# Optimization experiments

Measured on AMD Instinct MI355X. Metric: run time of the kernel, lower is better.

## Reference

```python
import jax, jax.numpy as jnp
import numpy as np

N, D, H = 100000, 128, 8
C = D // H
E = 800000
NEG_SLOPE = 0.2


def setup_inputs() -> dict:
    key = jax.random.key(0)
    k1, k2, k3, k4, k5, k6 = jax.random.split(key, 6)
    x = jax.random.normal(k1, (N, D), dtype=jnp.float32)
    edge_index = jax.random.randint(k2, (2, E), 0, N, dtype=jnp.int64)
    # GATConv params: shared linear (single node-feature input), per-head attention vectors, bias
    W = jax.random.normal(k3, (D, H * C), dtype=jnp.float32) * (1.0 / np.sqrt(D))
    att_src = jax.random.normal(k4, (H, C), dtype=jnp.float32) * 0.1
    att_dst = jax.random.normal(k5, (H, C), dtype=jnp.float32) * 0.1
    bias = jnp.zeros((H * C,), dtype=jnp.float32)
    return {"x": x, "edge_index": edge_index, "W": W, "att_src": att_src, "att_dst": att_dst, "bias": bias}


def reference(x, edge_index, W, att_src, att_dst, bias):
    # PyG GATConv default: add self-loops
    loops = jnp.tile(jnp.arange(N, dtype=edge_index.dtype), (2, 1))  # [2, N]
    ei = jnp.concatenate([edge_index, loops], axis=1)                # [2, E+N]
    src, dst = ei[0], ei[1]

    h = (x @ W).reshape(N, H, C)                    # [N, H, C]
    a_src = jnp.einsum('nhc,hc->nh', h, att_src)    # [N, H]
    a_dst = jnp.einsum('nhc,hc->nh', h, att_dst)    # [N, H]

    logits = jax.nn.leaky_relu(a_src[src] + a_dst[dst], negative_slope=NEG_SLOPE)  # [Etot, H]

    # segment softmax grouped by destination node (every node has a self-loop -> non-empty)
    mx = jax.ops.segment_max(logits, dst, num_segments=N)   # [N, H]
    ex = jnp.exp(logits - mx[dst])                           # [Etot, H]
    denom = jax.ops.segment_sum(ex, dst, num_segments=N)    # [N, H]
    alpha = ex / (denom[dst] + 1e-16)                        # [Etot, H]

    msg = h[src] * alpha[:, :, None]                         # [Etot, H, C]
    out = jax.ops.segment_sum(msg, dst, num_segments=N)      # [N, H, C]
    out = out.reshape(N, H * C) + bias                       # concat heads
    return out, ei, alpha
```

## Files before the change

kernel.cpp:

```cpp
#include <hip/hip_runtime.h>
#include <hip/hip_bf16.h>
#include <cstdint>

#define N_NODES 100000
#define DIM 128
#define HEADS 8
#define CH 16
#define NEDGE 800000
#define ETOT (NEDGE + N_NODES)
#define NEG_SLOPE 0.2f
#define CAP 64
#define PRE 20

typedef __attribute__((ext_vector_type(8))) short bf16x8;
typedef __attribute__((ext_vector_type(4))) float f32x4;

__device__ __forceinline__ float leaky(float v) {
    return v >= 0.f ? v : NEG_SLOPE * v;
}

__device__ __forceinline__ void split2(float w, ushort& hi, ushort& lo) {
    __hip_bfloat16 bh = __float2bfloat16(w);
    float r = w - __bfloat162float(bh);
    __hip_bfloat16 bl = __float2bfloat16(r);
    hi = *(ushort*)&bh;
    lo = *(ushort*)&bl;
}

#define NCOLS 144
#define LDK   136
#define MT    128
#define EDGE_TPB 512
#define EDGE_BLOCKS ((ETOT + EDGE_TPB - 1) / EDGE_TPB)
#define GEMM_BLOCKS ((N_NODES + MT - 1) / MT)

__global__ __launch_bounds__(512, 4) void fused_kernel(
    const float* __restrict__ x, const float* __restrict__ W,
    const float* __restrict__ att_src, const float* __restrict__ att_dst,
    __hip_bfloat16* __restrict__ h, float* __restrict__ a_src,
    float* __restrict__ a_dst,
    const int* __restrict__ edge_index, float* __restrict__ ei_out,
    int* __restrict__ fill, int* __restrict__ ebuf)
{
    __shared__ ushort Whi[NCOLS * LDK];
    __shared__ ushort Wlo[NCOLS * LDK];
    const int tid = threadIdx.x;

    if (blockIdx.x < EDGE_BLOCKS) {
        const int e = blockIdx.x * EDGE_TPB + tid;
        if (e < ETOT) {
            int s, d;
            if (e < NEDGE) { s = edge_index[e]; d = edge_index[NEDGE + e]; }
            else           { s = d = e - NEDGE; }
            ei_out[e]        = (float)s;
            ei_out[ETOT + e] = (float)d;
            int pos = atomicAdd(&fill[d], 1);
            if (pos < CAP) ebuf[d * CAP + pos] = e;
        }
        return;
    }
    const int bid = blockIdx.x - EDGE_BLOCKS;

    {
        const int n  = tid >> 2;
        const int kq = (tid & 3) * 32;
        #pragma unroll
        for (int j = 0; j < 32; j += 2) {
            const int k = kq + j;
            float w0 = W[(size_t)k * DIM + n];
            float w1 = W[(size_t)(k + 1) * DIM + n];
            ushort h0, l0, h1, l1;
            split2(w0, h0, l0);
            split2(w1, h1, l1);
            *(uint*)&Whi[n * LDK + k] = (uint)h0 | ((uint)h1 << 16);
            *(uint*)&Wlo[n * LDK + k] = (uint)l0 | ((uint)l1 << 16);
        }
    }
    if (tid < 64) {
        const int t  = tid >> 2;
        const int kq = (tid & 3) * 32;
        const int hd = t & 7;
        const float* av = ((t < 8) ? att_src : att_dst) + hd * CH;
        float avr[CH];
        #pragma unroll
        for (int c = 0; c < CH; ++c) avr[c] = av[c];
        const int nrow = 128 + t;
        for (int j = 0; j < 32; j += 2) {
            const int k = kq + j;
            const float* wp0 = &W[(size_t)k * DIM + hd * CH];
            const float* wp1 = wp0 + DIM;
            float s0 = 0.f, s1 = 0.f;
            #pragma unroll
            for (int c = 0; c < CH; ++c) { s0 += wp0[c] * avr[c]; s1 += wp1[c] * avr[c]; }
            ushort h0, l0, h1, l1;
            split2(s0, h0, l0);
            split2(s1, h1, l1);
            *(uint*)&Whi[nrow * LDK + k] = (uint)h0 | ((uint)h1 << 16);
            *(uint*)&Wlo[nrow * LDK + k] = (uint)l0 | ((uint)l1 << 16);
        }
    }
    __syncthreads();

    const int w    = tid >> 6;
    const int lane = tid & 63;
    const int r    = lane & 15;
    const int g    = lane >> 4;
    const long arow = (long)bid * MT + w * 16 + r;
    const bool avalid = arow < N_NODES;

    f32x4 acc[9] = {};
    #pragma unroll
    for (int ks = 0; ks < 4; ++ks) {
        const int k0 = ks * 32 + g * 8;
        float xv[8];
        if (avalid) {
            *(float4*)&xv[0] = *(const float4*)&x[arow * DIM + k0];
            *(float4*)&xv[4] = *(const float4*)&x[arow * DIM + k0 + 4];
        } else {
            #pragma unroll
            for (int j = 0; j < 8; ++j) xv[j] = 0.f;
        }
        bf16x8 ahi, alo;
        #pragma unroll
        for (int j = 0; j < 8; ++j) {
            ushort hb, lb;
            split2(xv[j], hb, lb);
            ahi[j] = (short)hb;
            alo[j] = (short)lb;
        }
        #pragma unroll
        for (int nt = 0; nt < 9; ++nt) {
            const int nr = nt * 16 + r;
            bf16x8 bhi = *(const bf16x8*)&Whi[nr * LDK + k0];
            bf16x8 blo = *(const bf16x8*)&Wlo[nr * LDK + k0];
            acc[nt] = __builtin_amdgcn_mfma_f32_16x16x32_bf16(ahi, bhi, acc[nt], 0, 0, 0);
            acc[nt] = __builtin_amdgcn_mfma_f32_16x16x32_bf16(alo, bhi, acc[nt], 0, 0, 0);
            acc[nt] = __builtin_amdgcn_mfma_f32_16x16x32_bf16(ahi, blo, acc[nt], 0, 0, 0);
        }
    }

    const long orow0 = (long)bid * MT + w * 16 + g * 4;
    #pragma unroll
    for (int q = 0; q < 4; ++q) {
        const long orow = orow0 + q;
        if (orow < N_NODES) {
            #pragma unroll
            for (int nt = 0; nt < 8; ++nt)
                h[orow * DIM + nt * 16 + r] = __float2bfloat16(acc[nt][q]);
            const float av = acc[8][q];
            if (r < 8) a_src[orow * HEADS + r]       = av;
            else       a_dst[orow * HEADS + (r - 8)] = av;
        }
    }
}

__global__ __launch_bounds__(256, 8) void gather_kernel(
    const int* __restrict__ edge_index, const int* __restrict__ fill,
    const int* __restrict__ ebuf, const __hip_bfloat16* __restrict__ h,
    const float* __restrict__ a_src, const float* __restrict__ a_dst,
    const float* __restrict__ bias, float* __restrict__ alpha_out,
    float* __restrict__ out)
{
    const int tid  = threadIdx.x;
    const int lane = tid & 63;
    const int n    = blockIdx.x * 4 + (tid >> 6);
    const int head = lane >> 3, c = lane & 7;
    const int chb  = head * CH + c * 2;

    const int   dn = min(fill[n], CAP);
    const float ad = a_dst[(uint)n * HEADS + head];
    const int   e  = ebuf[(uint)n * CAP + lane];
    int s = 0;
    if (lane < dn) s = (e < NEDGE) ? edge_index[e] : e - NEDGE;

    const char* hb  = (const char*)h;
    const uint  cho = (uint)chb * 2u;
    const int npre = min(dn, PRE);
    unsigned hv[PRE];
    #pragma unroll
    for (int q = 0; q < PRE; ++q) {
        int sq = __shfl(s, q);
        if (q < npre)
            hv[q] = *(const unsigned*)(hb + ((uint)sq * 256u + cho));
    }

    const char* asb = (const char*)a_src;
    const uint  hdo = (uint)(head << 2);
    float lg[8];
    float m = -1e30f;
    #pragma unroll
    for (int k = 0; k < 8; ++k) {
        const int i = c + 8 * k;
        if (i < dn) {
            int si = __shfl(s, i);
            float as = *(const float*)(asb + ((uint)si * 32u + hdo));
            lg[k] = leaky(as + ad);
            m = fmaxf(m, lg[k]);
        }
    }
    #pragma unroll
    for (int off = 1; off < 8; off <<= 1)
        m = fmaxf(m, __shfl_xor(m, off));

    float ex[8];
    float dsum = 0.f;
    #pragma unroll
    for (int k = 0; k < 8; ++k) {
        const int i = c + 8 * k;
        if (i < dn) { ex[k] = __expf(lg[k] - m); dsum += ex[k]; }
    }
    #pragma unroll
    for (int off = 1; off < 8; off <<= 1)
        dsum += __shfl_xor(dsum, off);
    const float rdinv = 1.f / (dsum + 1e-16f);

    float ax = 0.f, ay = 0.f;
    #pragma unroll
    for (int q = 0; q < PRE; ++q) {
        if (q < npre) {
            float exq = __shfl(ex[q >> 3], head * 8 + (q & 7));
            ax += __uint_as_float(hv[q] << 16) * exq;
            ay += __uint_as_float(hv[q] & 0xffff0000u) * exq;
        }
    }
    for (int q = PRE; q < dn; ++q) {
        int sq = __shfl(s, q);
        unsigned hq = *(const unsigned*)(hb + ((uint)sq * 256u + cho));
        float asq = *(const float*)(asb + ((uint)sq * 32u + hdo));
        float exq = __expf(leaky(asq + ad) - m);
        ax += __uint_as_float(hq << 16) * exq;
        ay += __uint_as_float(hq & 0xffff0000u) * exq;
    }
    ax *= rdinv; ay *= rdinv;
    float2 b = *(const float2*)&bias[chb];
    float2 rr; rr.x = ax + b.x; rr.y = ay + b.y;
    *(float2*)&out[(uint)n * DIM + chb] = rr;

    #pragma unroll
    for (int k = 0; k < 8; ++k) {
        const int i = c + 8 * k;
        if (i < dn) {
            int ei = __shfl(e, i);
            alpha_out[(uint)ei * 8u + head] = ex[k] * rdinv;
        }
    }
}

extern "C" void kernel_launch(void* const* d_in, const int* in_sizes, int n_in,
                              void* d_out, int out_size, void* d_ws, size_t ws_size,
                              hipStream_t stream) {
    const float* x          = (const float*)d_in[0];
    const int*   edge_index = (const int*)d_in[1];
    const float* W          = (const float*)d_in[2];
    const float* att_src    = (const float*)d_in[3];
    const float* att_dst    = (const float*)d_in[4];
    const float* bias       = (const float*)d_in[5];

    float* out       = (float*)d_out;
    float* ei_out    = out + (size_t)N_NODES * DIM;
    float* alpha_out = ei_out + 2 * (size_t)ETOT;

    __hip_bfloat16* h = (__hip_bfloat16*)d_ws;
    float* a_src = (float*)(h + (size_t)N_NODES * DIM);
    float* a_dst = a_src + (size_t)N_NODES * HEADS;
    int*   fill  = (int*)(a_dst + (size_t)N_NODES * HEADS);
    int*   ebuf  = fill + N_NODES;

    hipMemsetAsync(fill, 0, (size_t)N_NODES * sizeof(int), stream);

    fused_kernel<<<EDGE_BLOCKS + GEMM_BLOCKS, 512, 0, stream>>>(
        x, W, att_src, att_dst, h, a_src, a_dst,
        edge_index, ei_out, fill, ebuf);
    gather_kernel<<<N_NODES / 4, 256, 0, stream>>>(edge_index, fill, ebuf, h,
                                                   a_src, a_dst, bias, alpha_out, out);
}
```

Before: 292.9 us.

## Fold edge bucketing into GEMM blocks to overlap atomics with W preprocessing

Removes the separate edge-processing blocks and has each GEMM block handle a contiguous chunk of up to three edges per thread. The edge loads and atomicAdd on fill are issued before the W split/transpose work and the ebuf stores are deferred until after it, so atomic latency is hidden behind the shared-memory setup. The diff also lowers the gather prefetch depth PRE from 20 to 16 and relaxes the gather kernel's launch bounds from 8 to 4 blocks. Each GEMM block now carries extra register state and edge work, which may lengthen its critical path or reduce occupancy.

```diff
diff --git a/kernel.cpp b/kernel.cpp
--- a/kernel.cpp
+++ b/kernel.cpp
@@ -10,7 +10,7 @@
 #define ETOT (NEDGE + N_NODES)
 #define NEG_SLOPE 0.2f
 #define CAP 64
-#define PRE 20
+#define PRE 16
 
 typedef __attribute__((ext_vector_type(8))) short bf16x8;
 typedef __attribute__((ext_vector_type(4))) float f32x4;
@@ -30,9 +30,8 @@
 #define NCOLS 144
 #define LDK   136
 #define MT    128
-#define EDGE_TPB 512
-#define EDGE_BLOCKS ((ETOT + EDGE_TPB - 1) / EDGE_TPB)
 #define GEMM_BLOCKS ((N_NODES + MT - 1) / MT)
+#define EPB  ((ETOT + GEMM_BLOCKS - 1) / GEMM_BLOCKS)
 
 __global__ __launch_bounds__(512, 4) void fused_kernel(
     const float* __restrict__ x, const float* __restrict__ W,
@@ -45,21 +44,27 @@
     __shared__ ushort Whi[NCOLS * LDK];
     __shared__ ushort Wlo[NCOLS * LDK];
     const int tid = threadIdx.x;
-
-    if (blockIdx.x < EDGE_BLOCKS) {
-        const int e = blockIdx.x * EDGE_TPB + tid;
+    const int bid = blockIdx.x;
+
+    int ee[3], es[3], ed[3];
+    #pragma unroll
+    for (int t = 0; t < 3; ++t) {
+        const int e = bid * EPB + t * 512 + tid;
+        ee[t] = e;
         if (e < ETOT) {
-            int s, d;
-            if (e < NEDGE) { s = edge_index[e]; d = edge_index[NEDGE + e]; }
-            else           { s = d = e - NEDGE; }
-            ei_out[e]        = (float)s;
-            ei_out[ETOT + e] = (float)d;
-            int pos = atomicAdd(&fill[d], 1);
-            if (pos < CAP) ebuf[d * CAP + pos] = e;
-        }
-        return;
-    }
-    const int bid = blockIdx.x - EDGE_BLOCKS;
+            if (e < NEDGE) { es[t] = edge_index[e]; ed[t] = edge_index[NEDGE + e]; }
+            else           { es[t] = ed[t] = e - NEDGE; }
+        }
+    }
+    int pos[3];
+    #pragma unroll
+    for (int t = 0; t < 3; ++t) {
+        if (ee[t] < ETOT) {
+            ei_out[ee[t]]        = (float)es[t];
+            ei_out[ETOT + ee[t]] = (float)ed[t];
+            pos[t] = atomicAdd(&fill[ed[t]], 1);
+        }
+    }
 
     {
         const int n  = tid >> 2;
@@ -99,6 +104,12 @@
             *(uint*)&Wlo[nrow * LDK + k] = (uint)l0 | ((uint)l1 << 16);
         }
     }
+
+    #pragma unroll
+    for (int t = 0; t < 3; ++t) {
+        if (ee[t] < ETOT && pos[t] < CAP)
+            ebuf[ed[t] * CAP + pos[t]] = ee[t];
+    }
     __syncthreads();
 
     const int w    = tid >> 6;
@@ -154,7 +165,7 @@
     }
 }
 
-__global__ __launch_bounds__(256, 8) void gather_kernel(
+__global__ __launch_bounds__(256, 4) void gather_kernel(
     const int* __restrict__ edge_index, const int* __restrict__ fill,
     const int* __restrict__ ebuf, const __hip_bfloat16* __restrict__ h,
     const float* __restrict__ a_src, const float* __restrict__ a_dst,
@@ -268,7 +279,7 @@
 
     hipMemsetAsync(fill, 0, (size_t)N_NODES * sizeof(int), stream);
 
-    fused_kernel<<<EDGE_BLOCKS + GEMM_BLOCKS, 512, 0, stream>>>(
+    fused_kernel<<<GEMM_BLOCKS, 512, 0, stream>>>(
         x, W, att_src, att_dst, h, a_src, a_dst,
         edge_index, ei_out, fill, ebuf);
     gather_kernel<<<N_NODES / 4, 256, 0, stream>>>(edge_index, fill, ebuf, h,
```

Result: no change. 294.9 us (+0.7%).
